# Optimization experiments

Measured on AMD Instinct MI355X. Metric: run time of the kernel, lower is better.

Reference implementation:

```python
import jax, jax.numpy as jnp
import numpy as np
from jax import lax

B, L, D, H, NW, NL = 4, 256, 768, 384, 4, 9
WINDOWS = (3, 5, 7, 9)


def setup_inputs() -> dict:
    key = jax.random.key(0)
    ks = jax.random.split(key, 12)
    s = 0.05
    return {
        "seq_out": jax.random.normal(ks[0], (B, L, D), jnp.float32),
        "valid_ids": jax.random.randint(ks[1], (B, L), 0, 2),
        "w_ih_f": jax.random.normal(ks[2], (NW, 4 * H, D), jnp.float32) * s,
        "w_hh_f": jax.random.normal(ks[3], (NW, 4 * H, H), jnp.float32) * s,
        "b_ih_f": jax.random.normal(ks[4], (NW, 4 * H), jnp.float32) * s,
        "b_hh_f": jax.random.normal(ks[5], (NW, 4 * H), jnp.float32) * s,
        "w_ih_b": jax.random.normal(ks[6], (NW, 4 * H, D), jnp.float32) * s,
        "w_hh_b": jax.random.normal(ks[7], (NW, 4 * H, H), jnp.float32) * s,
        "b_ih_b": jax.random.normal(ks[8], (NW, 4 * H), jnp.float32) * s,
        "b_hh_b": jax.random.normal(ks[9], (NW, 4 * H), jnp.float32) * s,
        "lin_w": jax.random.normal(ks[10], (NL, D), jnp.float32) * s,
        "lin_b": jnp.zeros((NL,), jnp.float32),
    }


def _lstm_last(win, mask, W_ih, W_hh, b, reverse):
    # invalid (out-of-range) steps leave the state untouched, so the final
    # carry equals the hidden state after the last valid step (PyTorch LSTM math).
    Bx, Lx, w, Dx = win.shape
    Hh = W_hh.shape[1]

    def step(carry, xm):
        h, c = carry
        x_t, m = xm  # [B,L,D], [L]
        gates = x_t @ W_ih.T + h @ W_hh.T + b  # [B,L,4H], gate order i,f,g,o
        i, f, g, o = jnp.split(gates, 4, axis=-1)
        i = jax.nn.sigmoid(i)
        f = jax.nn.sigmoid(f)
        g = jnp.tanh(g)
        o = jax.nn.sigmoid(o)
        c_new = f * c + i * g
        h_new = o * jnp.tanh(c_new)
        m3 = m[None, :, None]
        return (jnp.where(m3, h_new, h), jnp.where(m3, c_new, c)), None

    init = (jnp.zeros((Bx, Lx, Hh), win.dtype), jnp.zeros((Bx, Lx, Hh), win.dtype))
    (h, _), _ = lax.scan(step, init, (jnp.moveaxis(win, 2, 0), mask.T), reverse=reverse)
    return h


def _window_features(x, w, Wif, Whf, bf, Wib, Whb, bb):
    # Faithful vectorization of windows_sequence: the sorted index_list for
    # position i is the contiguous slice [max(0,i-w//2) .. min(L-1,i+w//2)].
    Bx, Lx, Dx = x.shape
    half = w // 2
    pos = jnp.arange(Lx)[:, None] + jnp.arange(-half, half + 1)[None, :]  # [L,w]
    mask = (pos >= 0) & (pos < Lx)
    idx = jnp.clip(pos, 0, Lx - 1)
    win = x[:, idx, :]  # [B,L,w,D]
    h_f = _lstm_last(win, mask, Wif, Whf, bf, reverse=False)  # fwd dir: last output
    h_b = _lstm_last(win, mask, Wib, Whb, bb, reverse=True)   # bwd dir over reversed window
    return jnp.concatenate([h_f, h_b], axis=-1)  # [B,L,D]


def _valid_scatter(x, valid_ids):
    # Left-pack tokens with valid_ids==1 (the nested Python scatter loop).
    Bx, Lx, Dx = x.shape
    v = valid_ids.astype(jnp.int32)
    dest = jnp.where(v == 1, jnp.cumsum(v, axis=1) - 1, Lx)  # invalid -> pad slot

    def pack(row_x, row_d):
        return jnp.zeros((Lx + 1, Dx), row_x.dtype).at[row_d].set(row_x)[:Lx]

    return jax.vmap(pack)(x, dest)


def reference(seq_out, valid_ids, w_ih_f, w_hh_f, b_ih_f, b_hh_f,
              w_ih_b, w_hh_b, b_ih_b, b_hh_b, lin_w, lin_b):
    x = _valid_scatter(seq_out, valid_ids)  # [B,L,D]; dropout is identity in eval
    locals_ = [
        _window_features(x, WINDOWS[i],
                         w_ih_f[i], w_hh_f[i], b_ih_f[i] + b_hh_f[i],
                         w_ih_b[i], w_hh_b[i], b_ih_b[i] + b_hh_b[i])
        for i in range(NW)
    ]
    muti = jnp.stack(locals_, axis=2)  # [B,L,NW,D]
    # dot-att: query is the (packed) sequence output itself
    attn = jax.nn.softmax(
        jnp.einsum('bld,blwd->blw', x, muti) / jnp.sqrt(jnp.float32(D)), axis=-1)
    local_feat = jnp.einsum('blw,blwd->bld', attn, muti)
    out = x + local_feat
    return out @ lin_w.T + lin_b  # logits [B,L,NL]
```

## Files before the change

### kernel.cpp

```cpp
#include <hip/hip_runtime.h>
#include <math.h>

#define LL 256
#define DD 768
#define HH 384
#define G4 1536
#define NWIN 4
#define NLIN 9
#define NPOS 1024
#define PROJ_N 12288

typedef __attribute__((ext_vector_type(8))) short short8;
typedef __attribute__((ext_vector_type(4))) short short4v;
typedef __attribute__((ext_vector_type(16))) float f32x16;

static __device__ __forceinline__ float bf2f(unsigned short u) {
    union { unsigned int i; float f; } v; v.i = ((unsigned int)u) << 16; return v.f;
}
static __device__ __forceinline__ unsigned short f2bf(float f) {
    unsigned int u = __float_as_uint(f);
    u += 0x7fff + ((u >> 16) & 1);
    return (unsigned short)(u >> 16);
}
static __device__ __forceinline__ float fsig(float x) {
    return __builtin_amdgcn_rcpf(1.f + __expf(-x));
}
static __device__ __forceinline__ float ftanh(float x) {
    return 1.f - 2.f * __builtin_amdgcn_rcpf(1.f + __expf(2.f * x));
}

__global__ void zero_f4(float4* __restrict__ p, int n4) {
    int i = blockIdx.x * blockDim.x + threadIdx.x;
    if (i < n4) p[i] = make_float4(0.f, 0.f, 0.f, 0.f);
}

__global__ void scatter_kernel(const float* __restrict__ seq,
                               const int* __restrict__ valid,
                               float* __restrict__ x,
                               unsigned short* __restrict__ xfrag) {
    const int b = blockIdx.x >> 5;
    const int chunk = blockIdx.x & 31;
    const int tid = threadIdx.x;
    __shared__ int vbuf[LL];
    __shared__ int dest[LL];
    vbuf[tid] = valid[b * LL + tid];
    __syncthreads();
    if (tid == 0) {
        int c = 0;
        for (int l = 0; l < LL; ++l) dest[l] = vbuf[l] ? c++ : -1;
    }
    __syncthreads();
    for (int l = chunk * 8; l < chunk * 8 + 8; ++l) {
        const int d = dest[l];
        if (d >= 0) {
            const float* src = seq + (size_t)(b * LL + l) * DD;
            float* dst = x + (size_t)(b * LL + d) * DD;
            for (int j = tid; j < DD / 4; j += 256)
                ((float4*)dst)[j] = ((const float4*)src)[j];
            const int pos = b * LL + d;
            const int pt = pos >> 5, pl = pos & 31;
            for (int j = tid; j < DD / 8; j += 256) {
                const float4 v0 = ((const float4*)src)[2 * j];
                const float4 v1 = ((const float4*)src)[2 * j + 1];
                short8 pv;
                pv[0] = (short)f2bf(v0.x); pv[1] = (short)f2bf(v0.y);
                pv[2] = (short)f2bf(v0.z); pv[3] = (short)f2bf(v0.w);
                pv[4] = (short)f2bf(v1.x); pv[5] = (short)f2bf(v1.y);
                pv[6] = (short)f2bf(v1.z); pv[7] = (short)f2bf(v1.w);
                *(short8*)(xfrag + ((size_t)(pt * 48 + (j >> 1)) * 512 + (pl + 32 * (j & 1)) * 8)) = pv;
            }
        }
    }
}

__global__ __launch_bounds__(256) void cast_frag(
        const float* __restrict__ srcF, const float* __restrict__ srcB,
        unsigned short* __restrict__ dst, int K) {
    __shared__ unsigned short lds[32 * 768];
    const int tid = threadIdx.x;
    const int vrow0 = blockIdx.x * 32;
    const int chain = vrow0 / G4;
    const int dir = chain >> 2, wi = chain & 3;
    const float* src = (dir ? srcB : srcF) + (size_t)(wi * G4 + (vrow0 % G4)) * K;
    const int total = 32 * K;
    for (int i = tid * 4; i < total; i += 1024) {
        const float4 v = *(const float4*)(src + i);
        lds[i + 0] = f2bf(v.x); lds[i + 1] = f2bf(v.y);
        lds[i + 2] = f2bf(v.z); lds[i + 3] = f2bf(v.w);
    }
    __syncthreads();
    const int nks = K >> 4;
    for (int slot = tid; slot < nks * 64; slot += 256) {
        const int ks = slot >> 6;
        const int lane = slot & 63;
        const int row = lane & 31;
        const int kb = ks * 16 + (lane >> 5) * 8;
        const short8 v = *(const short8*)&lds[row * K + kb];
        *(short8*)(dst + ((size_t)blockIdx.x * nks + ks) * 512 + lane * 8) = v;
    }
}

__global__ void bias_kernel(const float* __restrict__ bihf, const float* __restrict__ bhhf,
                            const float* __restrict__ bihb, const float* __restrict__ bhhb,
                            float* __restrict__ bias) {
    const int n = blockIdx.x * 256 + threadIdx.x;
    if (n >= PROJ_N) return;
    const int chain = n / G4, r = n % G4;
    const int dir = chain >> 2, wi = chain & 3;
    bias[n] = (dir ? bihb : bihf)[wi * G4 + r] + (dir ? bhhb : bhhf)[wi * G4 + r];
}

__global__ __launch_bounds__(256) void proj_mfma(
        const unsigned short* __restrict__ xf,
        const unsigned short* __restrict__ wf,
        const float* __restrict__ bias,
        unsigned short* __restrict__ proj) {
    __shared__ __align__(16) unsigned short st[4 * 4096];
    const int wv = threadIdx.x >> 6;
    const int lane = threadIdx.x & 63;
    const int colid = lane & 31, hq = lane >> 5;
    const int mtg = blockIdx.x & 7;
    const int cu = blockIdx.x >> 3;
    const int chain = cu / 12;
    const int us = cu % 12;

    const unsigned short* bP = wf + (size_t)((chain * 48 + wv * 12 + us) * 48) * 512 + lane * 8;
    const unsigned short* aP = xf + (size_t)(mtg * 4 * 48) * 512 + lane * 8;

    f32x16 acc[4] = {};
#pragma unroll 4
    for (int ks = 0; ks < 48; ++ks) {
        const short8 bv = *(const short8*)(bP + ks * 512);
        const short8 a0 = *(const short8*)(aP + (0 * 48 + ks) * 512);
        const short8 a1 = *(const short8*)(aP + (1 * 48 + ks) * 512);
        const short8 a2 = *(const short8*)(aP + (2 * 48 + ks) * 512);
        const short8 a3 = *(const short8*)(aP + (3 * 48 + ks) * 512);
        acc[0] = __builtin_amdgcn_mfma_f32_32x32x16_bf16(a0, bv, acc[0], 0, 0, 0);
        acc[1] = __builtin_amdgcn_mfma_f32_32x32x16_bf16(a1, bv, acc[1], 0, 0, 0);
        acc[2] = __builtin_amdgcn_mfma_f32_32x32x16_bf16(a2, bv, acc[2], 0, 0, 0);
        acc[3] = __builtin_amdgcn_mfma_f32_32x32x16_bf16(a3, bv, acc[3], 0, 0, 0);
    }
    const float bv = bias[chain * G4 + wv * HH + us * 32 + colid];
#pragma unroll
    for (int i = 0; i < 4; ++i) {
#pragma unroll
        for (int r = 0; r < 16; ++r) {
            const int row = (r & 3) + 8 * (r >> 2) + 4 * hq;
            st[i * 4096 + (row * 32 + colid) * 4 + wv] = f2bf(acc[i][r] + bv);
        }
    }
    __syncthreads();
#pragma unroll
    for (int j = 0; j < 8; ++j) {
        const int idx = j * 256 + threadIdx.x;
        const int i = idx >> 9, rem = idx & 511;
        const int pl = rem >> 4, q = rem & 15;
        const int pos = (mtg * 4 + i) * 32 + pl;
        *(int4*)(proj + (size_t)pos * PROJ_N + chain * G4 + us * 128 + q * 8) =
            ((const int4*)st)[idx];
    }
}

__global__ __launch_bounds__(768, 3) void lstm_fused(
        const unsigned short* __restrict__ Wf,
        const unsigned short* __restrict__ proj,
        unsigned short* __restrict__ hfin) {
    const int p = blockIdx.x & 3, sub = (blockIdx.x >> 2) & 1;
    const int slot = blockIdx.x >> 3;
    const int chainA[4] = {3, 7, 2, 6};
    const int chainB[4] = {0, 4, 1, 5};
    const int chain = (slot < 16) ? chainA[p] : chainB[p];
    const int pt = sub * 16 + (slot & 15);
    const int dir = chain >> 2, wi = chain & 3;
    const int w = 3 + 2 * wi, half = wi + 1;
    const int tid = threadIdx.x;
    const int lane = tid & 63, wv = tid >> 6;
    const int colid = lane & 31, hq = lane >> 5;
    const int uu = wv * 32 + colid;
    const int m0 = pt * 32, b = m0 >> 8, l0 = m0 & 255;

    __shared__ __align__(16) unsigned short Hlds[24 * 512];
    ((int4*)Hlds)[tid] = make_int4(0, 0, 0, 0);
    ((int4*)Hlds)[tid + 768] = make_int4(0, 0, 0, 0);
    float c[16];
#pragma unroll
    for (int r = 0; r < 16; ++r) c[r] = 0.f;

    int sb[16];
#pragma unroll
    for (int r = 0; r < 16; ++r) {
        const int row = (r & 3) + 8 * (r >> 2) + 4 * hq;
        sb[r] = l0 + row - half;
    }

    const unsigned short* projb = proj + (size_t)(b * LL) * PROJ_N + chain * G4 + uu * 4;
    const unsigned short* Wb = Wf + (size_t)((chain * 48 + wv) * 24) * 512 + lane * 8;
    const unsigned short* Alds = Hlds + lane * 8;
    const int ksp = uu >> 4, khp = (uu >> 3) & 1, jp = uu & 7;

    __syncthreads();

    for (int s = 0; s < w; ++s) {
        const int t = dir ? (w - 1 - s) : s;
        short4v pj[16];
#pragma unroll
        for (int r = 0; r < 16; ++r) {
            int src = sb[r] + t;
            src = src < 0 ? 0 : (src > LL - 1 ? LL - 1 : src);
            pj[r] = *(const short4v*)(projb + src * PROJ_N);
        }
        f32x16 acc0 = {}, acc1 = {}, acc2 = {}, acc3 = {};
        if (s > 0) {
#pragma unroll 4
            for (int ks = 0; ks < 24; ++ks) {
                const short8 av  = *(const short8*)(Alds + ks * 512);
                const short8 bv0 = *(const short8*)(Wb + (size_t)(0 * 288 + ks) * 512);
                const short8 bv1 = *(const short8*)(Wb + (size_t)(1 * 288 + ks) * 512);
                const short8 bv2 = *(const short8*)(Wb + (size_t)(2 * 288 + ks) * 512);
                const short8 bv3 = *(const short8*)(Wb + (size_t)(3 * 288 + ks) * 512);
                acc0 = __builtin_amdgcn_mfma_f32_32x32x16_bf16(av, bv0, acc0, 0, 0, 0);
                acc1 = __builtin_amdgcn_mfma_f32_32x32x16_bf16(av, bv1, acc1, 0, 0, 0);
                acc2 = __builtin_amdgcn_mfma_f32_32x32x16_bf16(av, bv2, acc2, 0, 0, 0);
                acc3 = __builtin_amdgcn_mfma_f32_32x32x16_bf16(av, bv3, acc3, 0, 0, 0);
            }
        }
        __syncthreads();

#pragma unroll
        for (int r = 0; r < 16; ++r) {
            const int row = (r & 3) + 8 * (r >> 2) + 4 * hq;
            const int src = sb[r] + t;
            if (src >= 0 && src < LL) {
                const float gi = acc0[r] + bf2f((unsigned short)pj[r][0]);
                const float gf = acc1[r] + bf2f((unsigned short)pj[r][1]);
                const float gg = acc2[r] + bf2f((unsigned short)pj[r][2]);
                const float go = acc3[r] + bf2f((unsigned short)pj[r][3]);
                c[r] = fsig(gf) * c[r] + fsig(gi) * ftanh(gg);
                Hlds[ksp * 512 + (row + 32 * khp) * 8 + jp] = f2bf(fsig(go) * ftanh(c[r]));
            }
        }
        __syncthreads();
    }

    unsigned short* ho = hfin + (size_t)chain * (NPOS * HH) + (size_t)pt * 12288;
    ((int4*)ho)[tid] = ((const int4*)Hlds)[tid];
    ((int4*)ho)[tid + 768] = ((const int4*)Hlds)[tid + 768];
}

static __device__ __forceinline__ float hfrag_get(const unsigned short* __restrict__ h,
                                                  int chain, int P, int c) {
    const size_t idx = (size_t)chain * (NPOS * HH)
        + (size_t)((P >> 5) * 24 + (c >> 4)) * 512
        + ((P & 31) + 32 * ((c >> 3) & 1)) * 8 + (c & 7);
    return bf2f(h[idx]);
}

__global__ __launch_bounds__(256) void attn_out_kernel(
        const float* __restrict__ x, const unsigned short* __restrict__ hout,
        const float* __restrict__ lin_w, const float* __restrict__ lin_b,
        float* __restrict__ out) {
    const int P = blockIdx.x;
    const int tid = threadIdx.x;
    const int lane = tid & 63, wid = tid >> 6;
    __shared__ float sc[NWIN][4];
    __shared__ float attn_s[NWIN];
    __shared__ float ov[DD];
    __shared__ float red[NLIN][4];
    const float inv_sqrt_d = 0.03608439182435161f;

    float xr[3];
#pragma unroll
    for (int j = 0; j < 3; ++j) xr[j] = x[(size_t)P * DD + tid + 256 * j];

#pragma unroll
    for (int wi = 0; wi < NWIN; ++wi) {
        float part = 0.f;
#pragma unroll
        for (int j = 0; j < 3; ++j) {
            const int col = tid + 256 * j;
            const float m = (col < HH) ? hfrag_get(hout, wi, P, col)
                                       : hfrag_get(hout, 4 + wi, P, col - HH);
            part = fmaf(xr[j], m, part);
        }
        for (int off = 32; off > 0; off >>= 1) part += __shfl_down(part, off);
        if (lane == 0) sc[wi][wid] = part;
    }
    __syncthreads();
    if (tid == 0) {
        float s[NWIN], mx = -1e30f;
        for (int wi = 0; wi < NWIN; ++wi) {
            s[wi] = (sc[wi][0] + sc[wi][1] + sc[wi][2] + sc[wi][3]) * inv_sqrt_d;
            mx = fmaxf(mx, s[wi]);
        }
        float denom = 0.f;
        for (int wi = 0; wi < NWIN; ++wi) { s[wi] = __expf(s[wi] - mx); denom += s[wi]; }
        for (int wi = 0; wi < NWIN; ++wi) attn_s[wi] = s[wi] / denom;
    }
    __syncthreads();
#pragma unroll
    for (int j = 0; j < 3; ++j) {
        const int col = tid + 256 * j;
        float lv = 0.f;
#pragma unroll
        for (int wi = 0; wi < NWIN; ++wi) {
            const float m = (col < HH) ? hfrag_get(hout, wi, P, col)
                                       : hfrag_get(hout, 4 + wi, P, col - HH);
            lv = fmaf(attn_s[wi], m, lv);
        }
        ov[col] = xr[j] + lv;
    }
    __syncthreads();
    for (int r = 0; r < NLIN; ++r) {
        float part = 0.f;
#pragma unroll
        for (int j = 0; j < 3; ++j) {
            const int col = tid + 256 * j;
            part = fmaf(ov[col], lin_w[r * DD + col], part);
        }
        for (int off = 32; off > 0; off >>= 1) part += __shfl_down(part, off);
        if (lane == 0) red[r][wid] = part;
    }
    __syncthreads();
    if (tid < NLIN)
        out[(size_t)P * NLIN + tid] = red[tid][0] + red[tid][1] + red[tid][2] + red[tid][3] + lin_b[tid];
}

extern "C" void kernel_launch(void* const* d_in, const int* in_sizes, int n_in,
                              void* d_out, int out_size, void* d_ws, size_t ws_size,
                              hipStream_t stream) {
    (void)in_sizes; (void)n_in; (void)out_size; (void)ws_size;
    const float* seq   = (const float*)d_in[0];
    const int*   valid = (const int*)d_in[1];
    const float* wih_f = (const float*)d_in[2];
    const float* whh_f = (const float*)d_in[3];
    const float* bih_f = (const float*)d_in[4];
    const float* bhh_f = (const float*)d_in[5];
    const float* wih_b = (const float*)d_in[6];
    const float* whh_b = (const float*)d_in[7];
    const float* bih_b = (const float*)d_in[8];
    const float* bhh_b = (const float*)d_in[9];
    const float* lin_w = (const float*)d_in[10];
    const float* lin_b = (const float*)d_in[11];
    float* out = (float*)d_out;

    float*          x     = (float*)d_ws;
    unsigned short* xfrag = (unsigned short*)(x + NPOS * DD);
    unsigned short* proj  = xfrag + (size_t)NPOS * DD;
    unsigned short* wfhh  = proj + (size_t)NPOS * PROJ_N;
    unsigned short* wfih  = wfhh + (size_t)4718592;
    unsigned short* hfin  = wfih + (size_t)9437184;
    float*          bias  = (float*)(hfin + (size_t)8 * NPOS * HH);

    zero_f4<<<(294912 + 255) / 256, 256, 0, stream>>>((float4*)x, 294912);
    scatter_kernel<<<128, 256, 0, stream>>>(seq, valid, x, xfrag);
    cast_frag<<<384, 256, 0, stream>>>(wih_f, wih_b, wfih, DD);
    cast_frag<<<384, 256, 0, stream>>>(whh_f, whh_b, wfhh, HH);
    bias_kernel<<<48, 256, 0, stream>>>(bih_f, bhh_f, bih_b, bhh_b, bias);
    proj_mfma<<<768, 256, 0, stream>>>(xfrag, wfih, bias, proj);
    lstm_fused<<<256, 768, 0, stream>>>(wfhh, proj, hfin);
    attn_out_kernel<<<NPOS, 256, 0, stream>>>(x, hfin, lin_w, lin_b, out);
}
```

Before: 319.5 us.

## Double-buffer LSTM state, prefetch MFMA operands, fuse bias, rewrite attention epilogue

```diff
diff --git a/kernel.cpp b/kernel.cpp
--- a/kernel.cpp
+++ b/kernel.cpp
@@ -9,6 +9,7 @@
 #define NLIN 9
 #define NPOS 1024
 #define PROJ_N 12288
+#define HSTRIDE 520
 
 typedef __attribute__((ext_vector_type(8))) short short8;
 typedef __attribute__((ext_vector_type(4))) short short4v;
@@ -36,7 +37,6 @@
 
 __global__ void scatter_kernel(const float* __restrict__ seq,
                                const int* __restrict__ valid,
-                               float* __restrict__ x,
                                unsigned short* __restrict__ xfrag) {
     const int b = blockIdx.x >> 5;
     const int chunk = blockIdx.x & 31;
@@ -54,9 +54,6 @@
         const int d = dest[l];
         if (d >= 0) {
             const float* src = seq + (size_t)(b * LL + l) * DD;
-            float* dst = x + (size_t)(b * LL + d) * DD;
-            for (int j = tid; j < DD / 4; j += 256)
-                ((float4*)dst)[j] = ((const float4*)src)[j];
             const int pos = b * LL + d;
             const int pt = pos >> 5, pl = pos & 31;
             for (int j = tid; j < DD / 8; j += 256) {
@@ -100,20 +97,11 @@
     }
 }
 
-__global__ void bias_kernel(const float* __restrict__ bihf, const float* __restrict__ bhhf,
-                            const float* __restrict__ bihb, const float* __restrict__ bhhb,
-                            float* __restrict__ bias) {
-    const int n = blockIdx.x * 256 + threadIdx.x;
-    if (n >= PROJ_N) return;
-    const int chain = n / G4, r = n % G4;
-    const int dir = chain >> 2, wi = chain & 3;
-    bias[n] = (dir ? bihb : bihf)[wi * G4 + r] + (dir ? bhhb : bhhf)[wi * G4 + r];
-}
-
 __global__ __launch_bounds__(256) void proj_mfma(
         const unsigned short* __restrict__ xf,
         const unsigned short* __restrict__ wf,
-        const float* __restrict__ bias,
+        const float* __restrict__ bihf, const float* __restrict__ bhhf,
+        const float* __restrict__ bihb, const float* __restrict__ bhhb,
         unsigned short* __restrict__ proj) {
     __shared__ __align__(16) unsigned short st[4 * 4096];
     const int wv = threadIdx.x >> 6;
@@ -123,24 +111,34 @@
     const int cu = blockIdx.x >> 3;
     const int chain = cu / 12;
     const int us = cu % 12;
+    const int dir = chain >> 2, wi = chain & 3;
 
     const unsigned short* bP = wf + (size_t)((chain * 48 + wv * 12 + us) * 48) * 512 + lane * 8;
     const unsigned short* aP = xf + (size_t)(mtg * 4 * 48) * 512 + lane * 8;
 
     f32x16 acc[4] = {};
-#pragma unroll 4
+    short8 bc, bn, ac[4], an[4];
+    bc = *(const short8*)(bP);
+#pragma unroll
+    for (int i = 0; i < 4; ++i) ac[i] = *(const short8*)(aP + (i * 48) * 512);
+#pragma unroll
     for (int ks = 0; ks < 48; ++ks) {
-        const short8 bv = *(const short8*)(bP + ks * 512);
-        const short8 a0 = *(const short8*)(aP + (0 * 48 + ks) * 512);
-        const short8 a1 = *(const short8*)(aP + (1 * 48 + ks) * 512);
-        const short8 a2 = *(const short8*)(aP + (2 * 48 + ks) * 512);
-        const short8 a3 = *(const short8*)(aP + (3 * 48 + ks) * 512);
-        acc[0] = __builtin_amdgcn_mfma_f32_32x32x16_bf16(a0, bv, acc[0], 0, 0, 0);
-        acc[1] = __builtin_amdgcn_mfma_f32_32x32x16_bf16(a1, bv, acc[1], 0, 0, 0);
-        acc[2] = __builtin_amdgcn_mfma_f32_32x32x16_bf16(a2, bv, acc[2], 0, 0, 0);
-        acc[3] = __builtin_amdgcn_mfma_f32_32x32x16_bf16(a3, bv, acc[3], 0, 0, 0);
-    }
-    const float bv = bias[chain * G4 + wv * HH + us * 32 + colid];
+        if (ks < 47) {
+            bn = *(const short8*)(bP + (ks + 1) * 512);
+#pragma unroll
+            for (int i = 0; i < 4; ++i)
+                an[i] = *(const short8*)(aP + (i * 48 + ks + 1) * 512);
+        }
+        acc[0] = __builtin_amdgcn_mfma_f32_32x32x16_bf16(ac[0], bc, acc[0], 0, 0, 0);
+        acc[1] = __builtin_amdgcn_mfma_f32_32x32x16_bf16(ac[1], bc, acc[1], 0, 0, 0);
+        acc[2] = __builtin_amdgcn_mfma_f32_32x32x16_bf16(ac[2], bc, acc[2], 0, 0, 0);
+        acc[3] = __builtin_amdgcn_mfma_f32_32x32x16_bf16(ac[3], bc, acc[3], 0, 0, 0);
+        bc = bn;
+#pragma unroll
+        for (int i = 0; i < 4; ++i) ac[i] = an[i];
+    }
+    const int br = wv * HH + us * 32 + colid;
+    const float bv = (dir ? bihb : bihf)[wi * G4 + br] + (dir ? bhhb : bhhf)[wi * G4 + br];
 #pragma unroll
     for (int i = 0; i < 4; ++i) {
 #pragma unroll
@@ -178,151 +176,218 @@
     const int colid = lane & 31, hq = lane >> 5;
     const int uu = wv * 32 + colid;
     const int m0 = pt * 32, b = m0 >> 8, l0 = m0 & 255;
-
-    __shared__ __align__(16) unsigned short Hlds[24 * 512];
-    ((int4*)Hlds)[tid] = make_int4(0, 0, 0, 0);
-    ((int4*)Hlds)[tid + 768] = make_int4(0, 0, 0, 0);
+    const bool interior = ((pt & 7) >= 1) && ((pt & 7) <= 6);
+
+    __shared__ __align__(16) unsigned short Hbuf[2][24 * HSTRIDE];
     float c[16];
 #pragma unroll
     for (int r = 0; r < 16; ++r) c[r] = 0.f;
-
-    int sb[16];
-#pragma unroll
-    for (int r = 0; r < 16; ++r) {
-        const int row = (r & 3) + 8 * (r >> 2) + 4 * hq;
-        sb[r] = l0 + row - half;
-    }
 
     const unsigned short* projb = proj + (size_t)(b * LL) * PROJ_N + chain * G4 + uu * 4;
     const unsigned short* Wb = Wf + (size_t)((chain * 48 + wv) * 24) * 512 + lane * 8;
-    const unsigned short* Alds = Hlds + lane * 8;
     const int ksp = uu >> 4, khp = (uu >> 3) & 1, jp = uu & 7;
-
-    __syncthreads();
+    const int hslot = ksp * HSTRIDE + khp * 256 + jp;
 
     for (int s = 0; s < w; ++s) {
         const int t = dir ? (w - 1 - s) : s;
-        short4v pj[16];
-#pragma unroll
-        for (int r = 0; r < 16; ++r) {
-            int src = sb[r] + t;
-            src = src < 0 ? 0 : (src > LL - 1 ? LL - 1 : src);
-            pj[r] = *(const short4v*)(projb + src * PROJ_N);
-        }
+        const int tmh = t - half;
+        unsigned short* cur = Hbuf[s & 1];
+        const unsigned short* prev = Hbuf[(s & 1) ^ 1];
+
         f32x16 acc0 = {}, acc1 = {}, acc2 = {}, acc3 = {};
         if (s > 0) {
-#pragma unroll 4
+            const unsigned short* Alds = prev + lane * 8;
+            short8 wc0, wc1, wc2, wc3, acur, wn0, wn1, wn2, wn3, anx;
+            acur = *(const short8*)(Alds);
+            wc0 = *(const short8*)(Wb + 0 * 288 * 512);
+            wc1 = *(const short8*)(Wb + 1 * 288 * 512);
+            wc2 = *(const short8*)(Wb + 2 * 288 * 512);
+            wc3 = *(const short8*)(Wb + 3 * 288 * 512);
+#pragma unroll
             for (int ks = 0; ks < 24; ++ks) {
-                const short8 av  = *(const short8*)(Alds + ks * 512);
-                const short8 bv0 = *(const short8*)(Wb + (size_t)(0 * 288 + ks) * 512);
-                const short8 bv1 = *(const short8*)(Wb + (size_t)(1 * 288 + ks) * 512);
-                const short8 bv2 = *(const short8*)(Wb + (size_t)(2 * 288 + ks) * 512);
-                const short8 bv3 = *(const short8*)(Wb + (size_t)(3 * 288 + ks) * 512);
-                acc0 = __builtin_amdgcn_mfma_f32_32x32x16_bf16(av, bv0, acc0, 0, 0, 0);
-                acc1 = __builtin_amdgcn_mfma_f32_32x32x16_bf16(av, bv1, acc1, 0, 0, 0);
-                acc2 = __builtin_amdgcn_mfma_f32_32x32x16_bf16(av, bv2, acc2, 0, 0, 0);
-                acc3 = __builtin_amdgcn_mfma_f32_32x32x16_bf16(av, bv3, acc3, 0, 0, 0);
+                if (ks < 23) {
+                    anx = *(const short8*)(Alds + (ks + 1) * HSTRIDE);
+                    wn0 = *(const short8*)(Wb + (0 * 288 + ks + 1) * 512);
+                    wn1 = *(const short8*)(Wb + (1 * 288 + ks + 1) * 512);
+                    wn2 = *(const short8*)(Wb + (2 * 288 + ks + 1) * 512);
+                    wn3 = *(const short8*)(Wb + (3 * 288 + ks + 1) * 512);
+                }
+                acc0 = __builtin_amdgcn_mfma_f32_32x32x16_bf16(acur, wc0, acc0, 0, 0, 0);
+                acc1 = __builtin_amdgcn_mfma_f32_32x32x16_bf16(acur, wc1, acc1, 0, 0, 0);
+                acc2 = __builtin_amdgcn_mfma_f32_32x32x16_bf16(acur, wc2, acc2, 0, 0, 0);
+                acc3 = __builtin_amdgcn_mfma_f32_32x32x16_bf16(acur, wc3, acc3, 0, 0, 0);
+                acur = anx; wc0 = wn0; wc1 = wn1; wc2 = wn2; wc3 = wn3;
             }
         }
+
+        if (interior) {
+#pragma unroll
+            for (int rc = 0; rc < 4; ++rc) {
+                short4v pj[4];
+#pragma unroll
+                for (int q = 0; q < 4; ++q) {
+                    const int row = 8 * rc + 4 * hq + q;
+                    pj[q] = *(const short4v*)(projb + (l0 + row + tmh) * PROJ_N);
+                }
+#pragma unroll
+                for (int q = 0; q < 4; ++q) {
+                    const int r = rc * 4 + q;
+                    const int row = 8 * rc + 4 * hq + q;
+                    const float gi = acc0[r] + bf2f((unsigned short)pj[q][0]);
+                    const float gf = acc1[r] + bf2f((unsigned short)pj[q][1]);
+                    const float gg = acc2[r] + bf2f((unsigned short)pj[q][2]);
+                    const float go = acc3[r] + bf2f((unsigned short)pj[q][3]);
+                    c[r] = fsig(gf) * c[r] + fsig(gi) * ftanh(gg);
+                    cur[hslot + row * 8] = f2bf(fsig(go) * ftanh(c[r]));
+                }
+            }
+        } else {
+#pragma unroll
+            for (int rc = 0; rc < 4; ++rc) {
+                short4v pj[4];
+#pragma unroll
+                for (int q = 0; q < 4; ++q) {
+                    const int row = 8 * rc + 4 * hq + q;
+                    int src = l0 + row + tmh;
+                    src = src < 0 ? 0 : (src > LL - 1 ? LL - 1 : src);
+                    pj[q] = *(const short4v*)(projb + src * PROJ_N);
+                }
+#pragma unroll
+                for (int q = 0; q < 4; ++q) {
+                    const int r = rc * 4 + q;
+                    const int row = 8 * rc + 4 * hq + q;
+                    const int src = l0 + row + tmh;
+                    unsigned short hv;
+                    if (src >= 0 && src < LL) {
+                        const float gi = acc0[r] + bf2f((unsigned short)pj[q][0]);
+                        const float gf = acc1[r] + bf2f((unsigned short)pj[q][1]);
+                        const float gg = acc2[r] + bf2f((unsigned short)pj[q][2]);
+                        const float go = acc3[r] + bf2f((unsigned short)pj[q][3]);
+                        c[r] = fsig(gf) * c[r] + fsig(gi) * ftanh(gg);
+                        hv = f2bf(fsig(go) * ftanh(c[r]));
+                    } else {
+                        hv = (s == 0) ? (unsigned short)0 : prev[hslot + row * 8];
+                    }
+                    cur[hslot + row * 8] = hv;
+                }
+            }
+        }
         __syncthreads();
-
-#pragma unroll
-        for (int r = 0; r < 16; ++r) {
-            const int row = (r & 3) + 8 * (r >> 2) + 4 * hq;
-            const int src = sb[r] + t;
-            if (src >= 0 && src < LL) {
-                const float gi = acc0[r] + bf2f((unsigned short)pj[r][0]);
-                const float gf = acc1[r] + bf2f((unsigned short)pj[r][1]);
-                const float gg = acc2[r] + bf2f((unsigned short)pj[r][2]);
-                const float go = acc3[r] + bf2f((unsigned short)pj[r][3]);
-                c[r] = fsig(gf) * c[r] + fsig(gi) * ftanh(gg);
-                Hlds[ksp * 512 + (row + 32 * khp) * 8 + jp] = f2bf(fsig(go) * ftanh(c[r]));
-            }
-        }
-        __syncthreads();
-    }
-
+    }
+
+    const unsigned short* fin = Hbuf[(w - 1) & 1];
     unsigned short* ho = hfin + (size_t)chain * (NPOS * HH) + (size_t)pt * 12288;
-    ((int4*)ho)[tid] = ((const int4*)Hlds)[tid];
-    ((int4*)ho)[tid + 768] = ((const int4*)Hlds)[tid + 768];
-}
-
-static __device__ __forceinline__ float hfrag_get(const unsigned short* __restrict__ h,
-                                                  int chain, int P, int c) {
-    const size_t idx = (size_t)chain * (NPOS * HH)
-        + (size_t)((P >> 5) * 24 + (c >> 4)) * 512
-        + ((P & 31) + 32 * ((c >> 3) & 1)) * 8 + (c & 7);
-    return bf2f(h[idx]);
-}
-
-__global__ __launch_bounds__(256) void attn_out_kernel(
-        const float* __restrict__ x, const unsigned short* __restrict__ hout,
+#pragma unroll
+    for (int i = tid; i < 1536; i += 768) {
+        const int ks = i >> 6, off = i & 63;
+        *(int4*)(ho + ks * 512 + off * 8) = *(const int4*)(fin + ks * HSTRIDE + off * 8);
+    }
+}
+
+__global__ __launch_bounds__(512) void attn_out_kernel(
+        const unsigned short* __restrict__ xfrag,
+        const unsigned short* __restrict__ hfin,
         const float* __restrict__ lin_w, const float* __restrict__ lin_b,
         float* __restrict__ out) {
-    const int P = blockIdx.x;
+    const int pt = blockIdx.x;
     const int tid = threadIdx.x;
-    const int lane = tid & 63, wid = tid >> 6;
-    __shared__ float sc[NWIN][4];
-    __shared__ float attn_s[NWIN];
-    __shared__ float ov[DD];
-    __shared__ float red[NLIN][4];
+    const int lane = tid & 63, wv = tid >> 6;
+    const int dir = wv >> 2, kr = wv & 3;
+    const int pos = lane & 31, kh = lane >> 5;
     const float inv_sqrt_d = 0.03608439182435161f;
 
-    float xr[3];
-#pragma unroll
-    for (int j = 0; j < 3; ++j) xr[j] = x[(size_t)P * DD + tid + 256 * j];
-
-#pragma unroll
-    for (int wi = 0; wi < NWIN; ++wi) {
-        float part = 0.f;
-#pragma unroll
-        for (int j = 0; j < 3; ++j) {
-            const int col = tid + 256 * j;
-            const float m = (col < HH) ? hfrag_get(hout, wi, P, col)
-                                       : hfrag_get(hout, 4 + wi, P, col - HH);
-            part = fmaf(xr[j], m, part);
-        }
-        for (int off = 32; off > 0; off >>= 1) part += __shfl_down(part, off);
-        if (lane == 0) sc[wi][wid] = part;
-    }
-    __syncthreads();
-    if (tid == 0) {
-        float s[NWIN], mx = -1e30f;
-        for (int wi = 0; wi < NWIN; ++wi) {
-            s[wi] = (sc[wi][0] + sc[wi][1] + sc[wi][2] + sc[wi][3]) * inv_sqrt_d;
+    __shared__ float scp[8][4][32];
+    __shared__ float attw[4][32];
+    __shared__ float redp[8][32][10];
+
+    const unsigned short* xb = xfrag + ((size_t)(pt * 48 + 24 * dir)) * 512 + lane * 8;
+    const unsigned short* hb0 = hfin + (size_t)(dir * 4) * (NPOS * HH) + (size_t)pt * 12288 + lane * 8;
+
+    float sc4[4] = {0.f, 0.f, 0.f, 0.f};
+#pragma unroll
+    for (int k = 0; k < 6; ++k) {
+        const int ks = kr * 6 + k;
+        const short8 xv = *(const short8*)(xb + ks * 512);
+        float xf[8];
+#pragma unroll
+        for (int j = 0; j < 8; ++j) xf[j] = bf2f((unsigned short)xv[j]);
+#pragma unroll
+        for (int wi = 0; wi < 4; ++wi) {
+            const short8 hv = *(const short8*)(hb0 + (size_t)wi * (NPOS * HH) + ks * 512);
+#pragma unroll
+            for (int j = 0; j < 8; ++j)
+                sc4[wi] = fmaf(xf[j], bf2f((unsigned short)hv[j]), sc4[wi]);
+        }
+    }
+#pragma unroll
+    for (int wi = 0; wi < 4; ++wi) sc4[wi] += __shfl_down(sc4[wi], 32);
+    if (lane < 32) {
+#pragma unroll
+        for (int wi = 0; wi < 4; ++wi) scp[wv][wi][pos] = sc4[wi];
+    }
+    __syncthreads();
+    if (tid < 32) {
+        float s[4], mx = -1e30f;
+#pragma unroll
+        for (int wi = 0; wi < 4; ++wi) {
+            float v = 0.f;
+#pragma unroll
+            for (int g = 0; g < 8; ++g) v += scp[g][wi][tid];
+            s[wi] = v * inv_sqrt_d;
             mx = fmaxf(mx, s[wi]);
         }
         float denom = 0.f;
-        for (int wi = 0; wi < NWIN; ++wi) { s[wi] = __expf(s[wi] - mx); denom += s[wi]; }
-        for (int wi = 0; wi < NWIN; ++wi) attn_s[wi] = s[wi] / denom;
-    }
-    __syncthreads();
-#pragma unroll
-    for (int j = 0; j < 3; ++j) {
-        const int col = tid + 256 * j;
-        float lv = 0.f;
-#pragma unroll
-        for (int wi = 0; wi < NWIN; ++wi) {
-            const float m = (col < HH) ? hfrag_get(hout, wi, P, col)
-                                       : hfrag_get(hout, 4 + wi, P, col - HH);
-            lv = fmaf(attn_s[wi], m, lv);
-        }
-        ov[col] = xr[j] + lv;
-    }
-    __syncthreads();
-    for (int r = 0; r < NLIN; ++r) {
-        float part = 0.f;
-#pragma unroll
-        for (int j = 0; j < 3; ++j) {
-            const int col = tid + 256 * j;
-            part = fmaf(ov[col], lin_w[r * DD + col], part);
-        }
-        for (int off = 32; off > 0; off >>= 1) part += __shfl_down(part, off);
-        if (lane == 0) red[r][wid] = part;
-    }
-    __syncthreads();
-    if (tid < NLIN)
-        out[(size_t)P * NLIN + tid] = red[tid][0] + red[tid][1] + red[tid][2] + red[tid][3] + lin_b[tid];
+#pragma unroll
+        for (int wi = 0; wi < 4; ++wi) { s[wi] = __expf(s[wi] - mx); denom += s[wi]; }
+        const float rd = __builtin_amdgcn_rcpf(denom);
+#pragma unroll
+        for (int wi = 0; wi < 4; ++wi) attw[wi][tid] = s[wi] * rd;
+    }
+    __syncthreads();
+
+    float aw[4];
+#pragma unroll
+    for (int wi = 0; wi < 4; ++wi) aw[wi] = attw[wi][pos];
+    float rp[9];
+#pragma unroll
+    for (int r = 0; r < 9; ++r) rp[r] = 0.f;
+#pragma unroll
+    for (int k = 0; k < 6; ++k) {
+        const int ks = kr * 6 + k;
+        const short8 xv = *(const short8*)(xb + ks * 512);
+        float ov[8];
+#pragma unroll
+        for (int j = 0; j < 8; ++j) ov[j] = bf2f((unsigned short)xv[j]);
+#pragma unroll
+        for (int wi = 0; wi < 4; ++wi) {
+            const short8 hv = *(const short8*)(hb0 + (size_t)wi * (NPOS * HH) + ks * 512);
+#pragma unroll
+            for (int j = 0; j < 8; ++j)
+                ov[j] = fmaf(aw[wi], bf2f((unsigned short)hv[j]), ov[j]);
+        }
+        const int dbase = dir * 384 + ks * 16 + kh * 8;
+#pragma unroll
+        for (int r = 0; r < 9; ++r) {
+            const float4 lw0 = *(const float4*)(lin_w + r * DD + dbase);
+            const float4 lw1 = *(const float4*)(lin_w + r * DD + dbase + 4);
+            rp[r] += ov[0] * lw0.x + ov[1] * lw0.y + ov[2] * lw0.z + ov[3] * lw0.w
+                   + ov[4] * lw1.x + ov[5] * lw1.y + ov[6] * lw1.z + ov[7] * lw1.w;
+        }
+    }
+#pragma unroll
+    for (int r = 0; r < 9; ++r) rp[r] += __shfl_down(rp[r], 32);
+    if (lane < 32) {
+#pragma unroll
+        for (int r = 0; r < 9; ++r) redp[wv][pos][r] = rp[r];
+    }
+    __syncthreads();
+    if (tid < 288) {
+        const int p2 = tid / 9, r = tid % 9;
+        float s = lin_b[r];
+#pragma unroll
+        for (int g = 0; g < 8; ++g) s += redp[g][p2][r];
+        out[(size_t)(pt * 32 + p2) * NLIN + r] = s;
+    }
 }
 
 extern "C" void kernel_launch(void* const* d_in, const int* in_sizes, int n_in,
@@ -343,20 +408,17 @@
     const float* lin_b = (const float*)d_in[11];
     float* out = (float*)d_out;
 
-    float*          x     = (float*)d_ws;
-    unsigned short* xfrag = (unsigned short*)(x + NPOS * DD);
+    unsigned short* xfrag = (unsigned short*)d_ws;
     unsigned short* proj  = xfrag + (size_t)NPOS * DD;
     unsigned short* wfhh  = proj + (size_t)NPOS * PROJ_N;
     unsigned short* wfih  = wfhh + (size_t)4718592;
     unsigned short* hfin  = wfih + (size_t)9437184;
-    float*          bias  = (float*)(hfin + (size_t)8 * NPOS * HH);
-
-    zero_f4<<<(294912 + 255) / 256, 256, 0, stream>>>((float4*)x, 294912);
-    scatter_kernel<<<128, 256, 0, stream>>>(seq, valid, x, xfrag);
+
+    zero_f4<<<(98304 + 255) / 256, 256, 0, stream>>>((float4*)xfrag, 98304);
+    scatter_kernel<<<128, 256, 0, stream>>>(seq, valid, xfrag);
     cast_frag<<<384, 256, 0, stream>>>(wih_f, wih_b, wfih, DD);
     cast_frag<<<384, 256, 0, stream>>>(whh_f, whh_b, wfhh, HH);
-    bias_kernel<<<48, 256, 0, stream>>>(bih_f, bhh_f, bih_b, bhh_b, bias);
-    proj_mfma<<<768, 256, 0, stream>>>(xfrag, wfih, bias, proj);
+    proj_mfma<<<768, 256, 0, stream>>>(xfrag, wfih, bih_f, bhh_f, bih_b, bhh_b, proj);
     lstm_fused<<<256, 768, 0, stream>>>(wfhh, proj, hfin);
-    attn_out_kernel<<<NPOS, 256, 0, stream>>>(x, hfin, lin_w, lin_b, out);
-}
+    attn_out_kernel<<<32, 512, 0, stream>>>(xfrag, hfin, lin_w, lin_b, out);
+}
```

Result: slower. 654.6 us (+104.9%).
